# Performance work log

Hardware: AMD Instinct MI355X
Metric: run time of the kernel (lower is better)

## Reference

```python
import jax, jax.numpy as jnp
import numpy as np

# Config matching init_kwargs / input_specs
B, S = 8, 1024          # sequences, uniform seq_len (cu_seqlens = arange*S)
H, KVH, D = 32, 8, 128  # GQA: 4 query heads per kv head
BS, BPB, NB = 16, 64, 512  # block_size, blocks per seq, total blocks
T = B * S
SCALE = 0.08838834764831845  # 1/sqrt(head_dim)


def setup_inputs() -> dict:
    key = jax.random.key(0)
    kq, kk, kv = jax.random.split(key, 3)
    q = jax.random.normal(kq, (T, H * D), dtype=jnp.float32)
    k = jax.random.normal(kk, (T, KVH * D), dtype=jnp.float32)
    v = jax.random.normal(kv, (T, KVH * D), dtype=jnp.float32)
    k_cache = jnp.zeros((NB, BS, KVH, D), dtype=jnp.float32)
    v_cache = jnp.zeros((NB, BS, KVH, D), dtype=jnp.float32)
    # Contiguous page assignment: seq b uses blocks [b*BPB, (b+1)*BPB)
    block_tables = jnp.arange(B * BPB, dtype=jnp.int32).reshape(B, BPB)
    # token (b, t) -> slot block_tables[b, t//BS]*BS + t%BS == global arange here
    slot_mapping = jnp.arange(T, dtype=jnp.int32)
    return {"q": q, "k": k, "v": v, "k_cache": k_cache, "v_cache": v_cache,
            "slot_mapping": slot_mapping, "block_tables": block_tables}


def reference(q, k, v, k_cache, v_cache, slot_mapping, block_tables):
    # [T, H*D] -> [T, H, D]
    q = q.reshape(T, H, D)
    k = k.reshape(T, KVH, D)
    v = v.reshape(T, KVH, D)

    # store_kvcache: scatter new K/V into paged cache via slot_mapping
    kc = k_cache.reshape(NB * BS, KVH, D).at[slot_mapping].set(k)
    vc = v_cache.reshape(NB * BS, KVH, D).at[slot_mapping].set(v)

    # gather pages per sequence: [B, BPB, BS, KVH, D] -> [B, S, KVH, D]
    kg = kc.reshape(NB, BS, KVH, D)[block_tables].reshape(B, S, KVH, D)
    vg = vc.reshape(NB, BS, KVH, D)[block_tables].reshape(B, S, KVH, D)

    # GQA: expand kv heads to query heads
    G = H // KVH
    kg = jnp.repeat(kg, G, axis=2)  # [B, S, H, D]
    vg = jnp.repeat(vg, G, axis=2)

    qb = q.reshape(B, S, H, D)
    scores = jnp.einsum('bqhd,bkhd->bhqk', qb, kg) * SCALE  # [B, H, S, S]
    causal = jnp.tril(jnp.ones((S, S), dtype=bool))
    scores = jnp.where(causal[None, None], scores, jnp.finfo(scores.dtype).min)
    probs = jax.nn.softmax(scores, axis=-1)
    o = jnp.einsum('bhqk,bkhd->bqhd', probs, vg)  # [B, S, H, D]
    return o.reshape(T, H * D)
```

## Files before the change

kernel.cpp:

```cpp
#include <hip/hip_runtime.h>
#include <hip/hip_bf16.h>


namespace {

constexpr int Bc = 8, Sc = 1024, Hc = 32, KVHc = 8, Dc = 128;
constexpr float SCALEc = 0.08838834764831845f;
constexpr int KVBLK = 64;
constexpr int NQB = 16;
constexpr int KD = KVHc * Dc;
constexpr int HD = Hc * Dc;

typedef __attribute__((ext_vector_type(8))) short bf16x8;
typedef __attribute__((ext_vector_type(16))) float f32x16;

__device__ __forceinline__ unsigned short f2bf(float f) {
  union { __hip_bfloat16 h; unsigned short u; } c;
  c.h = __float2bfloat16(f);
  return c.u;
}
__device__ __forceinline__ unsigned pack2(float a, float b) {
  return (unsigned)f2bf(a) | ((unsigned)f2bf(b) << 16);
}

template <int ST>
__device__ __forceinline__ f32x16 qk_sub(const unsigned short* KB,
                                         const bf16x8* qf, int q32, int hi) {
  f32x16 a;
#pragma unroll
  for (int i = 0; i < 16; ++i) a[i] = 0.f;
  const int key = ST * 32 + q32;
  const char* kb = (const char*)KB + key * 256;
  const int sw = (key & 15) << 4;
#pragma unroll
  for (int ks = 0; ks < 8; ++ks) {
    bf16x8 kf = *(const bf16x8*)(kb + ((ks * 32 + hi * 16) ^ sw));
    a = __builtin_amdgcn_mfma_f32_32x32x16_bf16(kf, qf[ks], a, 0, 0, 0);
  }
  return a;
}

template <int ST>
__device__ __forceinline__ void pv_sub(const unsigned short* VB,
                                       const f32x16& p, f32x16* acc,
                                       int q32, int hi) {
  unsigned cp[8];
#pragma unroll
  for (int j = 0; j < 8; ++j) cp[j] = pack2(p[2 * j], p[2 * j + 1]);
  unsigned x[8];
#pragma unroll
  for (int j = 0; j < 8; ++j) x[j] = (unsigned)__shfl_xor((int)cp[j], 32);
  union { bf16x8 v; unsigned u[4]; } f0, f1;
  f0.u[0] = hi ? x[2] : cp[0];
  f0.u[1] = hi ? x[3] : cp[1];
  f0.u[2] = hi ? cp[2] : x[0];
  f0.u[3] = hi ? cp[3] : x[1];
  f1.u[0] = hi ? x[6] : cp[4];
  f1.u[1] = hi ? x[7] : cp[5];
  f1.u[2] = hi ? cp[6] : x[4];
  f1.u[3] = hi ? cp[7] : x[5];
#pragma unroll
  for (int ks2 = 0; ks2 < 2; ++ks2) {
    const bf16x8 pa = ks2 ? f1.v : f0.v;
#pragma unroll
    for (int dt = 0; dt < 4; ++dt) {
      const int d = dt * 32 + q32;
      const bf16x8 vf = *(const bf16x8*)(
          (const char*)VB + d * 128 +
          ((ST * 64 + ks2 * 32 + hi * 16) ^ ((d & 7) << 4)));
      acc[dt] = __builtin_amdgcn_mfma_f32_32x32x16_bf16(vf, pa, acc[dt], 0, 0, 0);
    }
  }
}

__global__ __launch_bounds__(512, 1) void attn_fwd(
    const float* __restrict__ qg, const float* __restrict__ kg,
    const float* __restrict__ vg, float* __restrict__ out) {
  const int bid = blockIdx.x;
  const int qband = (NQB - 1) - (bid >> 6);
  const int kvh = bid & 7;
  const int b = (bid >> 3) & 7;

  const int tid = threadIdx.x;
  const int w = tid >> 6, l = tid & 63;
  const int q32 = l & 31, hi = l >> 5;
  const int h = kvh * 4 + (w >> 1);
  const int qbase = qband * 64 + (w & 1) * 32;
  const int stdiag = w & 1;
  const int ntile = qband + 1;

  __shared__ unsigned short Kl[2][KVBLK * Dc];
  __shared__ unsigned short Vt[2][Dc * KVBLK];

  const float* qb = qg + (size_t)(b * Sc + qbase + q32) * HD + h * Dc;
  bf16x8 qf[8];
#pragma unroll
  for (int ks = 0; ks < 8; ++ks) {
    const int d0 = ks * 16 + hi * 8;
    float4 x = *(const float4*)(qb + d0);
    float4 y = *(const float4*)(qb + d0 + 4);
    bf16x8 t;
    t[0] = (short)f2bf(x.x * SCALEc); t[1] = (short)f2bf(x.y * SCALEc);
    t[2] = (short)f2bf(x.z * SCALEc); t[3] = (short)f2bf(x.w * SCALEc);
    t[4] = (short)f2bf(y.x * SCALEc); t[5] = (short)f2bf(y.y * SCALEc);
    t[6] = (short)f2bf(y.z * SCALEc); t[7] = (short)f2bf(y.w * SCALEc);
    qf[ks] = t;
  }

  f32x16 acc[4];
#pragma unroll
  for (int dt = 0; dt < 4; ++dt)
#pragma unroll
    for (int i = 0; i < 16; ++i) acc[dt][i] = 0.f;
  float m = -1e30f, lsum = 0.f;

  const float* kb0 = kg + (size_t)(b * Sc) * KD + kvh * Dc;
  const float* vb0 = vg + (size_t)(b * Sc) * KD + kvh * Dc;

  const int krow = tid >> 3, kd0 = (tid & 7) * 16;
  const int vd = tid & 127, vk0 = (tid >> 7) * 16;

  float4 kreg[4];
  float vreg[16];

  auto LOAD = [&](int T) {
    const float* kp = kb0 + ((size_t)T * KVBLK + krow) * KD + kd0;
    kreg[0] = *(const float4*)(kp);
    kreg[1] = *(const float4*)(kp + 4);
    kreg[2] = *(const float4*)(kp + 8);
    kreg[3] = *(const float4*)(kp + 12);
    const float* vp = vb0 + ((size_t)T * KVBLK + vk0) * KD + vd;
#pragma unroll
    for (int j = 0; j < 16; ++j) vreg[j] = vp[(size_t)j * KD];
  };
  auto STORE = [&](int cb) {
    unsigned short* KB = Kl[cb];
    unsigned short* VB = Vt[cb];
    uint4 A, Bq;
    A.x = pack2(kreg[0].x, kreg[0].y); A.y = pack2(kreg[0].z, kreg[0].w);
    A.z = pack2(kreg[1].x, kreg[1].y); A.w = pack2(kreg[1].z, kreg[1].w);
    Bq.x = pack2(kreg[2].x, kreg[2].y); Bq.y = pack2(kreg[2].z, kreg[2].w);
    Bq.z = pack2(kreg[3].x, kreg[3].y); Bq.w = pack2(kreg[3].z, kreg[3].w);
    const int kbase = krow * 256, ksw = (krow & 15) << 4;
    *(uint4*)((char*)KB + kbase + ((kd0 * 2) ^ ksw)) = A;
    *(uint4*)((char*)KB + kbase + ((kd0 * 2 + 16) ^ ksw)) = Bq;
    uint4 C0, C1;
    C0.x = pack2(vreg[0], vreg[1]);   C0.y = pack2(vreg[2], vreg[3]);
    C0.z = pack2(vreg[4], vreg[5]);   C0.w = pack2(vreg[6], vreg[7]);
    C1.x = pack2(vreg[8], vreg[9]);   C1.y = pack2(vreg[10], vreg[11]);
    C1.z = pack2(vreg[12], vreg[13]); C1.w = pack2(vreg[14], vreg[15]);
    const int vbase = vd * 128, vsw = (vd & 7) << 4;
    *(uint4*)((char*)VB + vbase + ((vk0 * 2) ^ vsw)) = C0;
    *(uint4*)((char*)VB + vbase + ((vk0 * 2 + 16) ^ vsw)) = C1;
  };

  LOAD(0);
  STORE(0);
  if (ntile > 1) LOAD(1);
  __syncthreads();

  for (int t = 0; t < ntile; ++t) {
    const int cb = t & 1;
    if (t + 1 < ntile) {
      STORE(cb ^ 1);
      if (t + 2 < ntile) LOAD(t + 2);
    }
    const unsigned short* KB = Kl[cb];
    const unsigned short* VB = Vt[cb];
    const bool last = (t == ntile - 1);
    const bool has1 = !(last && stdiag == 0);

    __builtin_amdgcn_s_setprio(1);
    f32x16 p0 = qk_sub<0>(KB, qf, q32, hi);
    f32x16 p1;
    if (has1) {
      p1 = qk_sub<1>(KB, qf, q32, hi);
    } else {
#pragma unroll
      for (int i = 0; i < 16; ++i) p1[i] = -1e30f;
    }
    __builtin_amdgcn_s_setprio(0);

    if (last) {
      const int kmb = t * KVBLK + stdiag * 32 + 4 * hi - qbase - q32;
      if (stdiag == 0) {
#pragma unroll
        for (int i = 0; i < 16; ++i) {
          const int kl = (i & 3) + 8 * (i >> 2);
          if (kmb + kl > 0) p0[i] = -1e30f;
        }
      } else {
#pragma unroll
        for (int i = 0; i < 16; ++i) {
          const int kl = (i & 3) + 8 * (i >> 2);
          if (kmb + kl > 0) p1[i] = -1e30f;
        }
      }
    }

    float pm = fmaxf(p0[0], p1[0]);
#pragma unroll
    for (int i = 1; i < 16; ++i) pm = fmaxf(pm, fmaxf(p0[i], p1[i]));
    pm = fmaxf(pm, __shfl_xor(pm, 32));
    if (__any(pm > m + 8.0f)) {
      const float mn = fmaxf(m, pm);
      const float alpha = __expf(m - mn);
      m = mn;
      lsum *= alpha;
#pragma unroll
      for (int dt = 0; dt < 4; ++dt) acc[dt] *= alpha;
    }
    float se = 0.f;
#pragma unroll
    for (int i = 0; i < 16; ++i) { p0[i] = __expf(p0[i] - m); se += p0[i]; }
    if (has1) {
#pragma unroll
      for (int i = 0; i < 16; ++i) { p1[i] = __expf(p1[i] - m); se += p1[i]; }
    }
    se += __shfl_xor(se, 32);
    lsum += se;

    __builtin_amdgcn_s_setprio(1);
    pv_sub<0>(VB, p0, acc, q32, hi);
    if (has1) pv_sub<1>(VB, p1, acc, q32, hi);
    __builtin_amdgcn_s_setprio(0);

    __syncthreads();
  }

  const float rinv = 1.0f / lsum;
  float* ob = out + (size_t)(b * Sc + qbase + q32) * HD + h * Dc;
#pragma unroll
  for (int dt = 0; dt < 4; ++dt)
#pragma unroll
    for (int g = 0; g < 4; ++g) {
      float4 o;
      o.x = acc[dt][g * 4 + 0] * rinv;
      o.y = acc[dt][g * 4 + 1] * rinv;
      o.z = acc[dt][g * 4 + 2] * rinv;
      o.w = acc[dt][g * 4 + 3] * rinv;
      *(float4*)(ob + dt * 32 + g * 8 + hi * 4) = o;
    }
}

}

extern "C" void kernel_launch(void* const* d_in, const int* in_sizes, int n_in,
                              void* d_out, int out_size, void* d_ws, size_t ws_size,
                              hipStream_t stream) {
  const float* q = (const float*)d_in[0];
  const float* k = (const float*)d_in[1];
  const float* v = (const float*)d_in[2];
  float* out = (float*)d_out;
  dim3 grid(NQB * 64);
  attn_fwd<<<grid, dim3(512), 0, stream>>>(q, k, v, out);
}
```

Baseline: 162.5 us.

## Pair complementary causal query bands per block for balanced work, use permlane32 swap

Each block now processes two query bands, the j-th from the top and the j-th from the bottom, so every block runs exactly 17 KV tiles. This halves the grid to 512 blocks and removes the causal load imbalance and tail effects. Launch bounds are raised to 2 blocks per CU to allow co-residency. The cross-half P fragment exchange uses v_permlane32_swap instead of shuffles plus selects. In exchange, each block runs a longer serial chain and must reload Q and reset its accumulators mid-loop, and the tighter register budget risks spills.

```diff
diff --git a/kernel.cpp b/kernel.cpp
--- a/kernel.cpp
+++ b/kernel.cpp
@@ -7,9 +7,9 @@
 constexpr int Bc = 8, Sc = 1024, Hc = 32, KVHc = 8, Dc = 128;
 constexpr float SCALEc = 0.08838834764831845f;
 constexpr int KVBLK = 64;
-constexpr int NQB = 16;
 constexpr int KD = KVHc * Dc;
 constexpr int HD = Hc * Dc;
+constexpr int NT = 17;
 
 typedef __attribute__((ext_vector_type(8))) short bf16x8;
 typedef __attribute__((ext_vector_type(16))) float f32x16;
@@ -21,6 +21,9 @@
 }
 __device__ __forceinline__ unsigned pack2(float a, float b) {
   return (unsigned)f2bf(a) | ((unsigned)f2bf(b) << 16);
+}
+__device__ __forceinline__ void pl32swap(unsigned& a, unsigned& b) {
+  asm volatile("v_permlane32_swap_b32 %0, %1" : "+v"(a), "+v"(b));
 }
 
 template <int ST>
@@ -47,18 +50,13 @@
   unsigned cp[8];
 #pragma unroll
   for (int j = 0; j < 8; ++j) cp[j] = pack2(p[2 * j], p[2 * j + 1]);
-  unsigned x[8];
-#pragma unroll
-  for (int j = 0; j < 8; ++j) x[j] = (unsigned)__shfl_xor((int)cp[j], 32);
+  pl32swap(cp[0], cp[2]);
+  pl32swap(cp[1], cp[3]);
+  pl32swap(cp[4], cp[6]);
+  pl32swap(cp[5], cp[7]);
   union { bf16x8 v; unsigned u[4]; } f0, f1;
-  f0.u[0] = hi ? x[2] : cp[0];
-  f0.u[1] = hi ? x[3] : cp[1];
-  f0.u[2] = hi ? cp[2] : x[0];
-  f0.u[3] = hi ? cp[3] : x[1];
-  f1.u[0] = hi ? x[6] : cp[4];
-  f1.u[1] = hi ? x[7] : cp[5];
-  f1.u[2] = hi ? cp[6] : x[4];
-  f1.u[3] = hi ? cp[7] : x[5];
+  f0.u[0] = cp[0]; f0.u[1] = cp[1]; f0.u[2] = cp[2]; f0.u[3] = cp[3];
+  f1.u[0] = cp[4]; f1.u[1] = cp[5]; f1.u[2] = cp[6]; f1.u[3] = cp[7];
 #pragma unroll
   for (int ks2 = 0; ks2 < 2; ++ks2) {
     const bf16x8 pa = ks2 ? f1.v : f0.v;
@@ -73,39 +71,43 @@
   }
 }
 
-__global__ __launch_bounds__(512, 1) void attn_fwd(
+__global__ __launch_bounds__(512, 2) void attn_fwd(
     const float* __restrict__ qg, const float* __restrict__ kg,
     const float* __restrict__ vg, float* __restrict__ out) {
   const int bid = blockIdx.x;
-  const int qband = (NQB - 1) - (bid >> 6);
+  const int j   = bid >> 6;
   const int kvh = bid & 7;
-  const int b = (bid >> 3) & 7;
+  const int b   = (bid >> 3) & 7;
+  const int nA  = 16 - j;
 
   const int tid = threadIdx.x;
   const int w = tid >> 6, l = tid & 63;
   const int q32 = l & 31, hi = l >> 5;
   const int h = kvh * 4 + (w >> 1);
-  const int qbase = qband * 64 + (w & 1) * 32;
   const int stdiag = w & 1;
-  const int ntile = qband + 1;
+
+  int qbase = (15 - j) * 64 + (w & 1) * 32;
 
   __shared__ unsigned short Kl[2][KVBLK * Dc];
   __shared__ unsigned short Vt[2][Dc * KVBLK];
 
-  const float* qb = qg + (size_t)(b * Sc + qbase + q32) * HD + h * Dc;
   bf16x8 qf[8];
-#pragma unroll
-  for (int ks = 0; ks < 8; ++ks) {
-    const int d0 = ks * 16 + hi * 8;
-    float4 x = *(const float4*)(qb + d0);
-    float4 y = *(const float4*)(qb + d0 + 4);
-    bf16x8 t;
-    t[0] = (short)f2bf(x.x * SCALEc); t[1] = (short)f2bf(x.y * SCALEc);
-    t[2] = (short)f2bf(x.z * SCALEc); t[3] = (short)f2bf(x.w * SCALEc);
-    t[4] = (short)f2bf(y.x * SCALEc); t[5] = (short)f2bf(y.y * SCALEc);
-    t[6] = (short)f2bf(y.z * SCALEc); t[7] = (short)f2bf(y.w * SCALEc);
-    qf[ks] = t;
-  }
+  auto LOADQ = [&](int qb_) {
+    const float* qp = qg + (size_t)(b * Sc + qb_ + q32) * HD + h * Dc;
+#pragma unroll
+    for (int ks = 0; ks < 8; ++ks) {
+      const int d0 = ks * 16 + hi * 8;
+      float4 x = *(const float4*)(qp + d0);
+      float4 y = *(const float4*)(qp + d0 + 4);
+      bf16x8 t;
+      t[0] = (short)f2bf(x.x * SCALEc); t[1] = (short)f2bf(x.y * SCALEc);
+      t[2] = (short)f2bf(x.z * SCALEc); t[3] = (short)f2bf(x.w * SCALEc);
+      t[4] = (short)f2bf(y.x * SCALEc); t[5] = (short)f2bf(y.y * SCALEc);
+      t[6] = (short)f2bf(y.z * SCALEc); t[7] = (short)f2bf(y.w * SCALEc);
+      qf[ks] = t;
+    }
+  };
+  LOADQ(qbase);
 
   f32x16 acc[4];
 #pragma unroll
@@ -113,6 +115,22 @@
 #pragma unroll
     for (int i = 0; i < 16; ++i) acc[dt][i] = 0.f;
   float m = -1e30f, lsum = 0.f;
+
+  auto WRITEO = [&](int qb_) {
+    const float rinv = 1.0f / lsum;
+    float* ob = out + (size_t)(b * Sc + qb_ + q32) * HD + h * Dc;
+#pragma unroll
+    for (int dt = 0; dt < 4; ++dt)
+#pragma unroll
+      for (int g = 0; g < 4; ++g) {
+        float4 o;
+        o.x = acc[dt][g * 4 + 0] * rinv;
+        o.y = acc[dt][g * 4 + 1] * rinv;
+        o.z = acc[dt][g * 4 + 2] * rinv;
+        o.w = acc[dt][g * 4 + 3] * rinv;
+        *(float4*)(ob + dt * 32 + g * 8 + hi * 4) = o;
+      }
+  };
 
   const float* kb0 = kg + (size_t)(b * Sc) * KD + kvh * Dc;
   const float* vb0 = vg + (size_t)(b * Sc) * KD + kvh * Dc;
@@ -131,7 +149,7 @@
     kreg[3] = *(const float4*)(kp + 12);
     const float* vp = vb0 + ((size_t)T * KVBLK + vk0) * KD + vd;
 #pragma unroll
-    for (int j = 0; j < 16; ++j) vreg[j] = vp[(size_t)j * KD];
+    for (int jj = 0; jj < 16; ++jj) vreg[jj] = vp[(size_t)jj * KD];
   };
   auto STORE = [&](int cb) {
     unsigned short* KB = Kl[cb];
@@ -153,21 +171,34 @@
     *(uint4*)((char*)VB + vbase + ((vk0 * 2) ^ vsw)) = C0;
     *(uint4*)((char*)VB + vbase + ((vk0 * 2 + 16) ^ vsw)) = C1;
   };
+  auto KT = [&](int i) { return i < nA ? i : i - nA; };
 
   LOAD(0);
   STORE(0);
-  if (ntile > 1) LOAD(1);
+  LOAD(KT(1));
   __syncthreads();
 
-  for (int t = 0; t < ntile; ++t) {
-    const int cb = t & 1;
-    if (t + 1 < ntile) {
+  for (int i = 0; i < NT; ++i) {
+    const int cb = i & 1;
+    if (i + 1 < NT) {
       STORE(cb ^ 1);
-      if (t + 2 < ntile) LOAD(t + 2);
-    }
+      if (i + 2 < NT) LOAD(KT(i + 2));
+    }
+    if (i == nA) {
+      WRITEO(qbase);
+      qbase = j * 64 + (w & 1) * 32;
+      LOADQ(qbase);
+#pragma unroll
+      for (int dt = 0; dt < 4; ++dt)
+#pragma unroll
+        for (int z = 0; z < 16; ++z) acc[dt][z] = 0.f;
+      m = -1e30f;
+      lsum = 0.f;
+    }
+    const int kt = KT(i);
     const unsigned short* KB = Kl[cb];
     const unsigned short* VB = Vt[cb];
-    const bool last = (t == ntile - 1);
+    const bool last = (i == nA - 1) || (i == NT - 1);
     const bool has1 = !(last && stdiag == 0);
 
     __builtin_amdgcn_s_setprio(1);
@@ -177,30 +208,30 @@
       p1 = qk_sub<1>(KB, qf, q32, hi);
     } else {
 #pragma unroll
-      for (int i = 0; i < 16; ++i) p1[i] = -1e30f;
+      for (int i2 = 0; i2 < 16; ++i2) p1[i2] = -1e30f;
     }
     __builtin_amdgcn_s_setprio(0);
 
     if (last) {
-      const int kmb = t * KVBLK + stdiag * 32 + 4 * hi - qbase - q32;
+      const int kmb = kt * KVBLK + stdiag * 32 + 4 * hi - qbase - q32;
       if (stdiag == 0) {
 #pragma unroll
-        for (int i = 0; i < 16; ++i) {
-          const int kl = (i & 3) + 8 * (i >> 2);
-          if (kmb + kl > 0) p0[i] = -1e30f;
+        for (int i2 = 0; i2 < 16; ++i2) {
+          const int kl = (i2 & 3) + 8 * (i2 >> 2);
+          if (kmb + kl > 0) p0[i2] = -1e30f;
         }
       } else {
 #pragma unroll
-        for (int i = 0; i < 16; ++i) {
-          const int kl = (i & 3) + 8 * (i >> 2);
-          if (kmb + kl > 0) p1[i] = -1e30f;
+        for (int i2 = 0; i2 < 16; ++i2) {
+          const int kl = (i2 & 3) + 8 * (i2 >> 2);
+          if (kmb + kl > 0) p1[i2] = -1e30f;
         }
       }
     }
 
     float pm = fmaxf(p0[0], p1[0]);
 #pragma unroll
-    for (int i = 1; i < 16; ++i) pm = fmaxf(pm, fmaxf(p0[i], p1[i]));
+    for (int i2 = 1; i2 < 16; ++i2) pm = fmaxf(pm, fmaxf(p0[i2], p1[i2]));
     pm = fmaxf(pm, __shfl_xor(pm, 32));
     if (__any(pm > m + 8.0f)) {
       const float mn = fmaxf(m, pm);
@@ -212,10 +243,10 @@
     }
     float se = 0.f;
 #pragma unroll
-    for (int i = 0; i < 16; ++i) { p0[i] = __expf(p0[i] - m); se += p0[i]; }
+    for (int i2 = 0; i2 < 16; ++i2) { p0[i2] = __expf(p0[i2] - m); se += p0[i2]; }
     if (has1) {
 #pragma unroll
-      for (int i = 0; i < 16; ++i) { p1[i] = __expf(p1[i] - m); se += p1[i]; }
+      for (int i2 = 0; i2 < 16; ++i2) { p1[i2] = __expf(p1[i2] - m); se += p1[i2]; }
     }
     se += __shfl_xor(se, 32);
     lsum += se;
@@ -228,19 +259,7 @@
     __syncthreads();
   }
 
-  const float rinv = 1.0f / lsum;
-  float* ob = out + (size_t)(b * Sc + qbase + q32) * HD + h * Dc;
-#pragma unroll
-  for (int dt = 0; dt < 4; ++dt)
-#pragma unroll
-    for (int g = 0; g < 4; ++g) {
-      float4 o;
-      o.x = acc[dt][g * 4 + 0] * rinv;
-      o.y = acc[dt][g * 4 + 1] * rinv;
-      o.z = acc[dt][g * 4 + 2] * rinv;
-      o.w = acc[dt][g * 4 + 3] * rinv;
-      *(float4*)(ob + dt * 32 + g * 8 + hi * 4) = o;
-    }
+  WRITEO(qbase);
 }
 
 }
@@ -252,6 +271,6 @@
   const float* k = (const float*)d_in[1];
   const float* v = (const float*)d_in[2];
   float* out = (float*)d_out;
-  dim3 grid(NQB * 64);
+  dim3 grid(512);
   attn_fwd<<<grid, dim3(512), 0, stream>>>(q, k, v, out);
 }
```

After: 155.3 us. 4.4% less time.
